# Optimization experiments

Measured on AMD Instinct MI355X. Metric: run time of the kernel, lower is better.

## Reference

```python
import jax, jax.numpy as jnp
import numpy as np
import math

N, M_KV = 8192, 8192
QDIM, KDIM, MID = 256, 256, 128
NEG_BIG = -float(1 << 32)  # matches torch.masked_fill(Attn, mask, -(1 << 32))


def setup_inputs() -> dict:
    key = jax.random.key(0)
    ks = jax.random.split(key, 8)
    main_feat = jax.random.normal(ks[0], (N, QDIM), dtype=jnp.float32)
    other_feat = jax.random.normal(ks[1], (M_KV, KDIM), dtype=jnp.float32)
    fix_feat = jax.random.uniform(ks[2], (M_KV,), dtype=jnp.float32)
    mask = jax.random.randint(ks[3], (N, M_KV), 0, 2).astype(jnp.bool_)
    # Linear params (torch.nn.Linear stores weight as [out, in])
    Wq = jax.random.normal(ks[4], (MID, QDIM), dtype=jnp.float32) / math.sqrt(QDIM)
    bq = jax.random.normal(ks[5], (MID,), dtype=jnp.float32) * 0.01
    Wk = jax.random.normal(ks[6], (MID, KDIM), dtype=jnp.float32) / math.sqrt(KDIM)
    bk = jax.random.normal(ks[7], (MID,), dtype=jnp.float32) * 0.01
    return {"main_feat": main_feat, "other_feat": other_feat, "fix_feat": fix_feat,
            "mask": mask, "Wq": Wq, "bq": bq, "Wk": Wk, "bk": bk}


def reference(main_feat, other_feat, fix_feat, mask, Wq, bq, Wk, bk):
    # Projections: y = x @ W.T + b
    Q = main_feat @ Wq.T + bq            # [N, MID]
    K = other_feat @ Wk.T + bk           # [M, MID]
    scale = 1.0 / math.sqrt(MID)
    attn = jnp.einsum('nd,md->nm', Q, K) * scale   # [N, M]
    attn = jnp.where(mask, NEG_BIG, attn)
    attn = jax.nn.softmax(attn, axis=-1)
    # diag(fix_feat) @ other_feat is just a row-wise scale of V
    V = fix_feat[:, None] * other_feat   # [M, KDIM]
    return attn @ V                      # [N, KDIM]
```

## Files before the change

### kernel.cpp

```cpp
#include <hip/hip_runtime.h>
#include <hip/hip_bf16.h>
#include <stdint.h>

typedef __attribute__((ext_vector_type(8))) short short8;
typedef __attribute__((ext_vector_type(4))) float floatx4;

#define MFMA32K(a, b, c) __builtin_amdgcn_mfma_f32_16x16x32_bf16(a, b, c, 0, 0, 0)

constexpr int N_Q  = 8192;
constexpr int M_KV = 8192;
constexpr int DMID = 128;
constexpr int DV   = 256;
constexpr int MWORDS = M_KV / 64;

__device__ __forceinline__ unsigned short f2bf(float x) {
    unsigned u = __float_as_uint(x);
    u += 0x7fffu + ((u >> 16) & 1u);
    return (unsigned short)(u >> 16);
}

__device__ __forceinline__ short8 cvt_f8_bf8(float4 a, float4 b) {
    short8 r;
    r[0] = (short)f2bf(a.x); r[1] = (short)f2bf(a.y);
    r[2] = (short)f2bf(a.z); r[3] = (short)f2bf(a.w);
    r[4] = (short)f2bf(b.x); r[5] = (short)f2bf(b.y);
    r[6] = (short)f2bf(b.z); r[7] = (short)f2bf(b.w);
    return r;
}

__device__ __forceinline__ void gl_lds16(const unsigned short* g, unsigned short* l) {
    __builtin_amdgcn_global_load_lds(
        (const __attribute__((address_space(1))) unsigned int*)g,
        (__attribute__((address_space(3))) unsigned int*)l, 16, 0, 0);
}

__device__ __forceinline__ unsigned nz4(unsigned x) {
    unsigned nz = (((x & 0x7f7f7f7fu) + 0x7f7f7f7fu) | x) & 0x80808080u;
    unsigned a = (nz >> 7) & 0x01010101u;
    return (a * 0x01020408u) >> 24;
}

__global__ void detect_mask_kernel(const unsigned int* __restrict__ mw, int* __restrict__ flag) {
    int t = threadIdx.x;
    unsigned w = mw[t];
    bool isf = (w == 0x3f800000u);
    bool isb = (w > 1u) && !isf;
    unsigned long long bf = __ballot(isf);
    unsigned long long bb = __ballot(isb);
    if (t == 0) *flag = bf ? 2 : (bb ? 1 : 0);
}

__global__ __launch_bounds__(256) void pack_mask_kernel(
    const void* __restrict__ mask, const int* __restrict__ flagp,
    unsigned long long* __restrict__ Mb)
{
    const int tid = threadIdx.x;
    const int f = *flagp;
    const int wbase = blockIdx.x * 256;
    const int wv = tid >> 6, lane = tid & 63;

    if (f == 1) {
        __shared__ unsigned short pbuf[1024];
        const uint4* g = (const uint4*)((const unsigned char*)mask + (size_t)wbase * 64);
#pragma unroll
        for (int r = 0; r < 4; ++r) {
            int p = wv * 256 + r * 64 + lane;
            uint4 v = g[p];
            unsigned m16 = nz4(v.x) | (nz4(v.y) << 4) | (nz4(v.z) << 8) | (nz4(v.w) << 12);
            pbuf[p] = (unsigned short)m16;
        }
        __syncthreads();
        Mb[wbase + tid] = ((const unsigned long long*)pbuf)[tid];
    } else {
        const unsigned int* mp = (const unsigned int*)mask;
        const int w0 = wbase + wv * 64;
#pragma unroll 4
        for (int i = 0; i < 64; ++i) {
            unsigned v = mp[(size_t)(w0 + i) * 64 + lane];
            unsigned long long b = __ballot(v != 0u);
            if (lane == 0) Mb[w0 + i] = b;
        }
    }
}

__global__ __launch_bounds__(256) void proj_kernel(
    const float* __restrict__ main_feat, const float* __restrict__ Wq, const float* __restrict__ bq,
    const float* __restrict__ other_feat, const float* __restrict__ Wk, const float* __restrict__ bk,
    unsigned short* __restrict__ Qw, unsigned short* __restrict__ Kw)
{
    const float* src;  const float* W;  const float* bias;  unsigned short* dst;
    if (blockIdx.y == 0) { src = main_feat;  W = Wq; bias = bq; dst = Qw; }
    else                 { src = other_feat; W = Wk; bias = bk; dst = Kw; }

    const int wave = threadIdx.x >> 6, lane = threadIdx.x & 63;
    const int n = lane & 15, quad = lane >> 4;
    const int row0 = blockIdx.x * 64 + wave * 16;

    short8 a[8];
    const float* ap = src + (size_t)(row0 + n) * 256 + quad * 8;
#pragma unroll
    for (int ks = 0; ks < 8; ++ks) {
        float4 x0 = *(const float4*)(ap + ks * 32);
        float4 x1 = *(const float4*)(ap + ks * 32 + 4);
        a[ks] = cvt_f8_bf8(x0, x1);
    }

    floatx4 acc[8];
#pragma unroll
    for (int nt = 0; nt < 8; ++nt) acc[nt] = floatx4{0.f, 0.f, 0.f, 0.f};

#pragma unroll
    for (int nt = 0; nt < 8; ++nt) {
        const float* wp = W + (size_t)(nt * 16 + n) * 256 + quad * 8;
#pragma unroll
        for (int ks = 0; ks < 8; ++ks) {
            float4 w0 = *(const float4*)(wp + ks * 32);
            float4 w1 = *(const float4*)(wp + ks * 32 + 4);
            short8 b = cvt_f8_bf8(w0, w1);
            acc[nt] = MFMA32K(a[ks], b, acc[nt]);
        }
    }

#pragma unroll
    for (int nt = 0; nt < 8; ++nt) {
        float bb = bias[nt * 16 + n];
#pragma unroll
        for (int reg = 0; reg < 4; ++reg) {
            int r = row0 + quad * 4 + reg;
            int c = nt * 16 + n;
            int phys = ((((c >> 3) + r) & 15) << 3) | (c & 7);
            dst[(size_t)r * DMID + phys] = f2bf(acc[nt][reg] + bb);
        }
    }
}

__global__ __launch_bounds__(256) void build_vt_kernel(
    const float* __restrict__ other_feat, const float* __restrict__ fix_feat,
    unsigned short* __restrict__ Vt)
{
    __shared__ unsigned short tile[64 * 72];
    const int t = threadIdx.x;
    const int m0 = blockIdx.x * 64, d0 = blockIdx.y * 64;

#pragma unroll
    for (int r = 0; r < 4; ++r) {
        int idx = r * 256 + t;
        int ml = idx >> 4, dl4 = (idx & 15) * 4;
        float4 v = *(const float4*)(other_feat + (size_t)(m0 + ml) * 256 + d0 + dl4);
        float f = fix_feat[m0 + ml];
        tile[(dl4 + 0) * 72 + ml] = f2bf(v.x * f);
        tile[(dl4 + 1) * 72 + ml] = f2bf(v.y * f);
        tile[(dl4 + 2) * 72 + ml] = f2bf(v.z * f);
        tile[(dl4 + 3) * 72 + ml] = f2bf(v.w * f);
    }
    __syncthreads();
#pragma unroll
    for (int r = 0; r < 8; ++r) {
        int dl = r * 8 + (t >> 5);
        int d = d0 + dl;
        int ml = (t & 31) * 2;
        int e = ml >> 5, s = (ml >> 4) & 1, q = (ml >> 2) & 3, j = ml & 3;
        int pc = e * 32 + q * 8 + s * 4 + j;
        int phys = ((((pc >> 3) + d) & 7) << 3) | (pc & 7);
        unsigned int v0 = tile[dl * 72 + ml];
        unsigned int v1 = tile[dl * 72 + ml + 1];
        *(unsigned int*)(Vt + (size_t)d * M_KV + m0 + phys) = v0 | (v1 << 16);
    }
}

__global__ __launch_bounds__(256, 2) void flash_kernel(
    const unsigned short* __restrict__ Qw, const unsigned short* __restrict__ Kw,
    const unsigned short* __restrict__ Vt, const unsigned long long* __restrict__ Mb,
    unsigned short* __restrict__ Opart, float* __restrict__ Lpart,
    int nsplit, int lgNs)
{
    __shared__ __align__(16) unsigned short k_lds[64 * 128];
    __shared__ __align__(16) unsigned short vt_lds[256 * 64];

    const int L = blockIdx.x + gridDim.x * blockIdx.y;
    const int ly = L & (nsplit - 1);
    const int lx = L >> lgNs;
    const int chunkLen = M_KV >> lgNs;
    const int mBeg = ly * chunkLen;
    const int tid = threadIdx.x;
    const int wave = tid >> 6, lane = tid & 63, n = lane & 15, quad = lane >> 4;
    const int qrow0 = lx * 128 + wave * 32;
    constexpr float SC = 0.08838834764831845f * 1.4426950408889634f;

    short8 qf[2][4];
#pragma unroll
    for (int qt = 0; qt < 2; ++qt)
#pragma unroll
        for (int db = 0; db < 4; ++db) {
            int row = qrow0 + qt * 16 + n;
            int phys = (db * 4 + quad + row) & 15;
            qf[qt][db] = *(const short8*)(Qw + (size_t)row * DMID + phys * 8);
        }

    floatx4 Oacc[2][16];
#pragma unroll
    for (int qt = 0; qt < 2; ++qt)
#pragma unroll
        for (int dt = 0; dt < 16; ++dt) Oacc[qt][dt] = floatx4{0.f, 0.f, 0.f, 0.f};

    float lrow[2] = {0.f, 0.f};

    const unsigned short* kg = Kw + (size_t)(wave * 4 + (lane >> 4)) * DMID + (lane & 15) * 8;
    const unsigned short* vg = Vt + (size_t)(wave * 8 + (lane >> 3)) * M_KV + (lane & 7) * 8;
    unsigned short* kld = &k_lds[wave * 512];
    unsigned short* vld = &vt_lds[wave * 512];
    const int kqn = quad + n;

    const int iters = chunkLen / 64;
    for (int it = 0; it < iters; ++it) {
        const int m0 = mBeg + it * 64;
        __syncthreads();
#pragma unroll
        for (int r = 0; r < 4; ++r)
            gl_lds16(kg + (size_t)(m0 + r * 16) * DMID, kld + r * 2048);
#pragma unroll
        for (int r = 0; r < 8; ++r)
            gl_lds16(vg + (size_t)(r * 32) * M_KV + m0, vld + r * 2048);
        unsigned long long wbits[2];
#pragma unroll
        for (int qt = 0; qt < 2; ++qt)
            wbits[qt] = Mb[(size_t)(qrow0 + qt * 16 + n) * MWORDS + (m0 >> 6)];
        __syncthreads();

        floatx4 ST[4][2];
#pragma unroll
        for (int kvt = 0; kvt < 4; ++kvt) {
            const int rowoff = (kvt * 16 + n) * DMID;
            short8 a0 = *(const short8*)&k_lds[rowoff + (((kqn + 0) & 15) << 3)];
            short8 a1 = *(const short8*)&k_lds[rowoff + (((kqn + 4) & 15) << 3)];
            short8 a2 = *(const short8*)&k_lds[rowoff + (((kqn + 8) & 15) << 3)];
            short8 a3 = *(const short8*)&k_lds[rowoff + (((kqn + 12) & 15) << 3)];
#pragma unroll
            for (int qt = 0; qt < 2; ++qt) {
                floatx4 s = floatx4{0.f, 0.f, 0.f, 0.f};
                s = MFMA32K(a0, qf[qt][0], s);
                s = MFMA32K(a1, qf[qt][1], s);
                s = MFMA32K(a2, qf[qt][2], s);
                s = MFMA32K(a3, qf[qt][3], s);
                ST[kvt][qt] = s;
            }
        }

        short8 pf8[2][2];
#pragma unroll
        for (int qt = 0; qt < 2; ++qt) {
            unsigned long long x = wbits[qt] >> (quad * 4);
            float lacc = 0.f;
#pragma unroll
            for (int kvt = 0; kvt < 4; ++kvt) {
                int e = kvt >> 1, s = kvt & 1;
                float p[4];
#pragma unroll
                for (int j = 0; j < 4; ++j) {
                    float v = __builtin_amdgcn_exp2f(ST[kvt][qt][j] * SC);
                    p[j] = ((x >> (kvt * 16 + j)) & 1ull) ? 0.f : v;
                    lacc += p[j];
                }
                __hip_bfloat162 h0 = __float22bfloat162_rn(make_float2(p[0], p[1]));
                __hip_bfloat162 h1 = __float22bfloat162_rn(make_float2(p[2], p[3]));
                unsigned u0, u1;
                __builtin_memcpy(&u0, &h0, 4);
                __builtin_memcpy(&u1, &h1, 4);
                ((unsigned*)&pf8[qt][e])[s * 2 + 0] = u0;
                ((unsigned*)&pf8[qt][e])[s * 2 + 1] = u1;
            }
            lrow[qt] += lacc;
        }

#pragma unroll
        for (int e = 0; e < 2; ++e) {
#pragma unroll
            for (int dt = 0; dt < 16; ++dt) {
                const int vb = (dt * 16 + n) * 64 + (((e * 4 + quad + n) & 7) << 3);
                short8 bv = *(const short8*)&vt_lds[vb];
                Oacc[0][dt] = MFMA32K(pf8[0][e], bv, Oacc[0][dt]);
                Oacc[1][dt] = MFMA32K(pf8[1][e], bv, Oacc[1][dt]);
            }
        }
    }

    const size_t obase = (size_t)ly * N_Q * DV;
#pragma unroll
    for (int qt = 0; qt < 2; ++qt)
#pragma unroll
        for (int dt = 0; dt < 16; ++dt)
#pragma unroll
            for (int reg = 0; reg < 4; ++reg) {
                int gr = qrow0 + qt * 16 + quad * 4 + reg;
                Opart[obase + (size_t)gr * DV + dt * 16 + n] = f2bf(Oacc[qt][dt][reg]);
            }
#pragma unroll
    for (int qt = 0; qt < 2; ++qt) {
        float r = lrow[qt];
        r += __shfl_xor(r, 16);
        r += __shfl_xor(r, 32);
        if (quad == 0)
            Lpart[ly * N_Q + qrow0 + qt * 16 + n] = r;
    }
}

__global__ __launch_bounds__(256) void combine_kernel(
    const unsigned short* __restrict__ Opart, const float* __restrict__ Lpart,
    float* __restrict__ out, int nsplit)
{
    const int row = blockIdx.x, d = threadIdx.x;
    float L = 0.f, o = 0.f;
    for (int c = 0; c < nsplit; ++c) {
        L += Lpart[c * N_Q + row];
        unsigned int b = Opart[((size_t)c * N_Q + row) * DV + d];
        o += __uint_as_float(b << 16);
    }
    out[(size_t)row * DV + d] = o / L;
}

extern "C" void kernel_launch(void* const* d_in, const int* in_sizes, int n_in,
                              void* d_out, int out_size, void* d_ws, size_t ws_size,
                              hipStream_t stream)
{
    const float* main_feat  = (const float*)d_in[0];
    const float* other_feat = (const float*)d_in[1];
    const float* fix_feat   = (const float*)d_in[2];
    const void*  mask       = d_in[3];
    const float* Wq         = (const float*)d_in[4];
    const float* bq         = (const float*)d_in[5];
    const float* Wk         = (const float*)d_in[6];
    const float* bk         = (const float*)d_in[7];
    float* out = (float*)d_out;

    char* ws = (char*)d_ws;
    unsigned short* Qw = (unsigned short*)(ws);
    unsigned short* Kw = (unsigned short*)(ws + (1ull << 21));
    unsigned short* Vt = (unsigned short*)(ws + (2ull << 21));
    int* flag = (int*)(ws + (8ull << 20));
    unsigned long long* Mb = (unsigned long long*)(ws + (8ull << 20) + 1024);
    float* Lpart = (float*)(ws + (16ull << 20) + 2048);

    const size_t base = (16ull << 20) + 2048;
    auto need = [&](int ns) {
        return base + (size_t)ns * N_Q * 4 + (size_t)ns * N_Q * DV * 2;
    };
    int nsplit = 1, lgNs = 0;
    if (ws_size >= need(8))      { nsplit = 8; lgNs = 3; }
    else if (ws_size >= need(4)) { nsplit = 4; lgNs = 2; }
    else if (ws_size >= need(2)) { nsplit = 2; lgNs = 1; }

    unsigned short* Opart = (unsigned short*)(Lpart + (size_t)nsplit * N_Q);

    hipLaunchKernelGGL(detect_mask_kernel, dim3(1), dim3(64), 0, stream,
                       (const unsigned int*)mask, flag);
    hipLaunchKernelGGL(pack_mask_kernel, dim3(N_Q * MWORDS / 256), dim3(256), 0, stream,
                       mask, flag, Mb);
    hipLaunchKernelGGL(proj_kernel, dim3(128, 2), dim3(256), 0, stream,
                       main_feat, Wq, bq, other_feat, Wk, bk, Qw, Kw);
    hipLaunchKernelGGL(build_vt_kernel, dim3(128, 4), dim3(256), 0, stream,
                       other_feat, fix_feat, Vt);
    hipLaunchKernelGGL(flash_kernel, dim3(64, nsplit), dim3(256), 0, stream,
                       Qw, Kw, Vt, Mb, Opart, Lpart, nsplit, lgNs);
    hipLaunchKernelGGL(combine_kernel, dim3(N_Q), dim3(256), 0, stream,
                       Opart, Lpart, out, nsplit);
}
```

Measured before the change: 497.3 us.

## Halve query rows per wave in flash kernel to raise occupancy

Each wave now processes one 16-row query tile instead of two. The block covers 64 query rows and the grid doubles along x, and launch bounds ask for 3 blocks per CU. This cuts accumulator registers so more waves can be resident to hide latency. In exchange, each K/V tile loaded into LDS and each V fragment read is reused over half as many query rows, which doubles K/V memory traffic.

```diff
diff --git a/kernel.cpp b/kernel.cpp
--- a/kernel.cpp
+++ b/kernel.cpp
@@ -168,7 +168,7 @@
     }
 }
 
-__global__ __launch_bounds__(256, 2) void flash_kernel(
+__global__ __launch_bounds__(256, 3) void flash_kernel(
     const unsigned short* __restrict__ Qw, const unsigned short* __restrict__ Kw,
     const unsigned short* __restrict__ Vt, const unsigned long long* __restrict__ Mb,
     unsigned short* __restrict__ Opart, float* __restrict__ Lpart,
@@ -178,32 +178,28 @@
     __shared__ __align__(16) unsigned short vt_lds[256 * 64];
 
     const int L = blockIdx.x + gridDim.x * blockIdx.y;
-    const int ly = L & (nsplit - 1);
+    const int chunk = L & (nsplit - 1);
     const int lx = L >> lgNs;
     const int chunkLen = M_KV >> lgNs;
-    const int mBeg = ly * chunkLen;
+    const int mBeg = chunk * chunkLen;
     const int tid = threadIdx.x;
     const int wave = tid >> 6, lane = tid & 63, n = lane & 15, quad = lane >> 4;
-    const int qrow0 = lx * 128 + wave * 32;
+    const int qrow0 = lx * 64 + wave * 16;
     constexpr float SC = 0.08838834764831845f * 1.4426950408889634f;
 
-    short8 qf[2][4];
-#pragma unroll
-    for (int qt = 0; qt < 2; ++qt)
-#pragma unroll
-        for (int db = 0; db < 4; ++db) {
-            int row = qrow0 + qt * 16 + n;
-            int phys = (db * 4 + quad + row) & 15;
-            qf[qt][db] = *(const short8*)(Qw + (size_t)row * DMID + phys * 8);
-        }
-
-    floatx4 Oacc[2][16];
-#pragma unroll
-    for (int qt = 0; qt < 2; ++qt)
-#pragma unroll
-        for (int dt = 0; dt < 16; ++dt) Oacc[qt][dt] = floatx4{0.f, 0.f, 0.f, 0.f};
-
-    float lrow[2] = {0.f, 0.f};
+    short8 qf[4];
+#pragma unroll
+    for (int db = 0; db < 4; ++db) {
+        int row = qrow0 + n;
+        int phys = (db * 4 + quad + row) & 15;
+        qf[db] = *(const short8*)(Qw + (size_t)row * DMID + phys * 8);
+    }
+
+    floatx4 Oacc[16];
+#pragma unroll
+    for (int dt = 0; dt < 16; ++dt) Oacc[dt] = floatx4{0.f, 0.f, 0.f, 0.f};
+
+    float lrow = 0.f;
 
     const unsigned short* kg = Kw + (size_t)(wave * 4 + (lane >> 4)) * DMID + (lane & 15) * 8;
     const unsigned short* vg = Vt + (size_t)(wave * 8 + (lane >> 3)) * M_KV + (lane & 7) * 8;
@@ -221,13 +217,10 @@
 #pragma unroll
         for (int r = 0; r < 8; ++r)
             gl_lds16(vg + (size_t)(r * 32) * M_KV + m0, vld + r * 2048);
-        unsigned long long wbits[2];
-#pragma unroll
-        for (int qt = 0; qt < 2; ++qt)
-            wbits[qt] = Mb[(size_t)(qrow0 + qt * 16 + n) * MWORDS + (m0 >> 6)];
+        unsigned long long wbits = Mb[(size_t)(qrow0 + n) * MWORDS + (m0 >> 6)];
         __syncthreads();
 
-        floatx4 ST[4][2];
+        floatx4 ST[4];
 #pragma unroll
         for (int kvt = 0; kvt < 4; ++kvt) {
             const int rowoff = (kvt * 16 + n) * DMID;
@@ -235,21 +228,17 @@
             short8 a1 = *(const short8*)&k_lds[rowoff + (((kqn + 4) & 15) << 3)];
             short8 a2 = *(const short8*)&k_lds[rowoff + (((kqn + 8) & 15) << 3)];
             short8 a3 = *(const short8*)&k_lds[rowoff + (((kqn + 12) & 15) << 3)];
-#pragma unroll
-            for (int qt = 0; qt < 2; ++qt) {
-                floatx4 s = floatx4{0.f, 0.f, 0.f, 0.f};
-                s = MFMA32K(a0, qf[qt][0], s);
-                s = MFMA32K(a1, qf[qt][1], s);
-                s = MFMA32K(a2, qf[qt][2], s);
-                s = MFMA32K(a3, qf[qt][3], s);
-                ST[kvt][qt] = s;
-            }
-        }
-
-        short8 pf8[2][2];
-#pragma unroll
-        for (int qt = 0; qt < 2; ++qt) {
-            unsigned long long x = wbits[qt] >> (quad * 4);
+            floatx4 s = floatx4{0.f, 0.f, 0.f, 0.f};
+            s = MFMA32K(a0, qf[0], s);
+            s = MFMA32K(a1, qf[1], s);
+            s = MFMA32K(a2, qf[2], s);
+            s = MFMA32K(a3, qf[3], s);
+            ST[kvt] = s;
+        }
+
+        short8 pf8[2];
+        {
+            unsigned long long x = wbits >> (quad * 4);
             float lacc = 0.f;
 #pragma unroll
             for (int kvt = 0; kvt < 4; ++kvt) {
@@ -257,7 +246,7 @@
                 float p[4];
 #pragma unroll
                 for (int j = 0; j < 4; ++j) {
-                    float v = __builtin_amdgcn_exp2f(ST[kvt][qt][j] * SC);
+                    float v = __builtin_amdgcn_exp2f(ST[kvt][j] * SC);
                     p[j] = ((x >> (kvt * 16 + j)) & 1ull) ? 0.f : v;
                     lacc += p[j];
                 }
@@ -266,10 +255,10 @@
                 unsigned u0, u1;
                 __builtin_memcpy(&u0, &h0, 4);
                 __builtin_memcpy(&u1, &h1, 4);
-                ((unsigned*)&pf8[qt][e])[s * 2 + 0] = u0;
-                ((unsigned*)&pf8[qt][e])[s * 2 + 1] = u1;
+                ((unsigned*)&pf8[e])[s * 2 + 0] = u0;
+                ((unsigned*)&pf8[e])[s * 2 + 1] = u1;
             }
-            lrow[qt] += lacc;
+            lrow += lacc;
         }
 
 #pragma unroll
@@ -278,29 +267,25 @@
             for (int dt = 0; dt < 16; ++dt) {
                 const int vb = (dt * 16 + n) * 64 + (((e * 4 + quad + n) & 7) << 3);
                 short8 bv = *(const short8*)&vt_lds[vb];
-                Oacc[0][dt] = MFMA32K(pf8[0][e], bv, Oacc[0][dt]);
-                Oacc[1][dt] = MFMA32K(pf8[1][e], bv, Oacc[1][dt]);
+                Oacc[dt] = MFMA32K(pf8[e], bv, Oacc[dt]);
             }
         }
     }
 
-    const size_t obase = (size_t)ly * N_Q * DV;
-#pragma unroll
-    for (int qt = 0; qt < 2; ++qt)
-#pragma unroll
-        for (int dt = 0; dt < 16; ++dt)
-#pragma unroll
-            for (int reg = 0; reg < 4; ++reg) {
-                int gr = qrow0 + qt * 16 + quad * 4 + reg;
-                Opart[obase + (size_t)gr * DV + dt * 16 + n] = f2bf(Oacc[qt][dt][reg]);
-            }
-#pragma unroll
-    for (int qt = 0; qt < 2; ++qt) {
-        float r = lrow[qt];
+    const size_t obase = (size_t)chunk * N_Q * DV;
+#pragma unroll
+    for (int dt = 0; dt < 16; ++dt)
+#pragma unroll
+        for (int reg = 0; reg < 4; ++reg) {
+            int gr = qrow0 + quad * 4 + reg;
+            Opart[obase + (size_t)gr * DV + dt * 16 + n] = f2bf(Oacc[dt][reg]);
+        }
+    {
+        float r = lrow;
         r += __shfl_xor(r, 16);
         r += __shfl_xor(r, 32);
         if (quad == 0)
-            Lpart[ly * N_Q + qrow0 + qt * 16 + n] = r;
+            Lpart[chunk * N_Q + qrow0 + n] = r;
     }
 }
 
@@ -359,7 +344,7 @@
                        main_feat, Wq, bq, other_feat, Wk, bk, Qw, Kw);
     hipLaunchKernelGGL(build_vt_kernel, dim3(128, 4), dim3(256), 0, stream,
                        other_feat, fix_feat, Vt);
-    hipLaunchKernelGGL(flash_kernel, dim3(64, nsplit), dim3(256), 0, stream,
+    hipLaunchKernelGGL(flash_kernel, dim3(128, nsplit), dim3(256), 0, stream,
                        Qw, Kw, Vt, Mb, Opart, Lpart, nsplit, lgNs);
     hipLaunchKernelGGL(combine_kernel, dim3(N_Q), dim3(256), 0, stream,
                        Opart, Lpart, out, nsplit);
```

New measurement: 520.3 us. 1.05x slower.
